# Optimization experiments

Hardware: AMD Instinct MI355X
Metric: run time of the kernel (lower is better)

## Reference

```python
import jax, jax.numpy as jnp
import numpy as np

D = 768
H = 8
HD = D // H
FF = 4 * D


def _linear_params(key, din, dout):
    kw, kb = jax.random.split(key)
    lim = 1.0 / np.sqrt(din)
    W = jax.random.uniform(kw, (din, dout), jnp.float32, -lim, lim)
    b = jax.random.uniform(kb, (dout,), jnp.float32, -lim, lim)
    return W, b


def setup_inputs() -> dict:
    key = jax.random.key(0)
    ks = jax.random.split(key, 8)
    x = jax.random.normal(ks[0], (16, 1024, D), jnp.float32)
    Wq, bq = _linear_params(ks[1], D, D)
    Wk, bk = _linear_params(ks[2], D, D)
    Wv, bv = _linear_params(ks[3], D, D)
    Wo, bo = _linear_params(ks[4], D, D)
    W1, b1 = _linear_params(ks[5], D, FF)
    W2, b2 = _linear_params(ks[6], FF, D)
    gamma = jnp.ones((D,), jnp.float32)
    beta = jnp.zeros((D,), jnp.float32)
    return {"x": x, "gamma": gamma, "beta": beta,
            "Wq": Wq, "bq": bq, "Wk": Wk, "bk": bk, "Wv": Wv, "bv": bv,
            "Wo": Wo, "bo": bo, "W1": W1, "b1": b1, "W2": W2, "b2": b2}


def _layernorm(x, gamma, beta, eps=1e-5):
    mu = jnp.mean(x, axis=-1, keepdims=True)
    var = jnp.var(x, axis=-1, keepdims=True)
    return (x - mu) * jax.lax.rsqrt(var + eps) * gamma + beta


def _block(x, gamma, beta, Wq, bq, Wk, bk, Wv, bv, Wo, bo, W1, b1, W2, b2):
    b, n, d = x.shape
    residual = x
    h = _layernorm(x, gamma, beta)
    # QKV projections -> [b, h, n, hd]
    q = (h @ Wq + bq).reshape(b, n, H, HD).transpose(0, 2, 1, 3)
    k = (h @ Wk + bk).reshape(b, n, H, HD).transpose(0, 2, 1, 3)
    v = (h @ Wv + bv).reshape(b, n, H, HD).transpose(0, 2, 1, 3)
    scale = HD ** 0.5
    scores = jnp.einsum('bhid,bhjd->bhij', q, k) / scale
    attn = jax.nn.softmax(scores, axis=-1)
    out = jnp.einsum('bhij,bhjd->bhid', attn, v)
    out = out.transpose(0, 2, 1, 3).reshape(b, n, d)
    out = out @ Wo + bo
    out = out + residual
    residual = out
    h = _layernorm(out, gamma, beta)  # same LN params reused (as in source)
    h = jax.nn.gelu(h @ W1 + b1, approximate=False)
    h = h @ W2 + b2
    return h + residual


def reference(x, gamma, beta, Wq, bq, Wk, bk, Wv, bv, Wo, bo, W1, b1, W2, b2):
    return _block(x, gamma, beta, Wq, bq, Wk, bk, Wv, bv, Wo, bo, W1, b1, W2, b2)
```

## Files before the change

kernel.cpp:

```cpp
#include <hip/hip_runtime.h>

typedef unsigned short u16;
typedef float f32x4 __attribute__((ext_vector_type(4)));
typedef __bf16 bf16x8 __attribute__((ext_vector_type(8)));

#define AS1 __attribute__((address_space(1)))
#define AS3 __attribute__((address_space(3)))

__device__ __forceinline__ float bf2f(u16 h) {
  return __uint_as_float(((unsigned)h) << 16);
}
__device__ __forceinline__ u16 f2bf(float f) {
  unsigned u = __float_as_uint(f);
  unsigned r = (u + 0x7FFFu + ((u >> 16) & 1u)) >> 16;
  return (u16)r;
}
__device__ __forceinline__ void gload16(const u16* g, u16* l) {
  __builtin_amdgcn_global_load_lds((const AS1 void*)g, (AS3 void*)l, 16, 0, 0);
}

__global__ void transpose_k(const float* __restrict__ in, u16* __restrict__ out,
                            int R, int C) {
  __shared__ u16 t[32][33];
  int c0 = blockIdx.x * 32, r0 = blockIdx.y * 32;
  int tx = threadIdx.x & 31, ty = threadIdx.x >> 5;
  for (int i = 0; i < 32; i += 8)
    t[ty + i][tx] = f2bf(in[(size_t)(r0 + ty + i) * C + c0 + tx]);
  __syncthreads();
  for (int i = 0; i < 32; i += 8)
    out[(size_t)(c0 + ty + i) * R + r0 + tx] = t[tx][ty + i];
}

__global__ void vtrans_k(const u16* __restrict__ v, u16* __restrict__ vt) {
  __shared__ u16 t[32][33];
  int bh = blockIdx.z, b = bh >> 3, h = bh & 7;
  int n0 = blockIdx.y * 32, d0 = blockIdx.x * 32;
  int tx = threadIdx.x & 31, ty = threadIdx.x >> 5;
  const u16* src = v + (size_t)(b * 1024) * 768 + h * 96;
  for (int i = 0; i < 32; i += 8)
    t[ty + i][tx] = src[(size_t)(n0 + ty + i) * 768 + d0 + tx];
  __syncthreads();
  u16* dst = vt + ((size_t)bh * 96 + d0) * 1024 + n0;
  for (int i = 0; i < 32; i += 8)
    dst[(size_t)(ty + i) * 1024 + tx] = t[tx][ty + i];
}

__global__ __launch_bounds__(256) void ln_f32_k(const float* __restrict__ x,
                                                const float* __restrict__ gamma,
                                                const float* __restrict__ beta,
                                                u16* __restrict__ out) {
  __shared__ float red[8];
  int row = blockIdx.x, t = threadIdx.x;
  const float* xr = x + (size_t)row * 768;
  float v[3], s = 0.f, s2 = 0.f;
#pragma unroll
  for (int i = 0; i < 3; i++) {
    v[i] = xr[t + i * 256];
    s += v[i]; s2 += v[i] * v[i];
  }
#pragma unroll
  for (int off = 1; off < 64; off <<= 1) {
    s += __shfl_xor(s, off, 64);
    s2 += __shfl_xor(s2, off, 64);
  }
  int w = t >> 6;
  if ((t & 63) == 0) { red[w] = s; red[4 + w] = s2; }
  __syncthreads();
  s = red[0] + red[1] + red[2] + red[3];
  s2 = red[4] + red[5] + red[6] + red[7];
  float mu = s * (1.f / 768.f);
  float var = s2 * (1.f / 768.f) - mu * mu;
  float rs = rsqrtf(var + 1e-5f);
  u16* orow = out + (size_t)row * 768;
#pragma unroll
  for (int i = 0; i < 3; i++) {
    int c = t + i * 256;
    orow[c] = f2bf((v[i] - mu) * rs * gamma[c] + beta[c]);
  }
}

#define BM 128
#define BN 128
#define BK 32

template <int EPI>
__global__ __launch_bounds__(256, 2) void gemm_bt(
    const u16* __restrict__ A, const u16* __restrict__ Bt,
    const float* __restrict__ bias, const float* __restrict__ res,
    void* __restrict__ Cv, int M, int N, int K) {
  __shared__ u16 As[BM * BK];
  __shared__ u16 Bs[BN * BK];
  int tid = threadIdx.x, lane = tid & 63, w = tid >> 6;
  int l15 = lane & 15, quad = lane >> 4;
  int wm = (w >> 1) * 64, wn = (w & 1) * 64;
  int m0 = blockIdx.x * BM, n0 = blockIdx.y * BN;
  f32x4 acc[4][4] = {};
  for (int k0 = 0; k0 < K; k0 += BK) {
    __syncthreads();
#pragma unroll
    for (int i = 0; i < 2; i++) {
      int c = w * 2 + i;
      int e = c * 512 + lane * 8;
      int r = e >> 5, col = e & 31;
      gload16(A + (size_t)(m0 + r) * K + k0 + col, As + c * 512);
      gload16(Bt + (size_t)(n0 + r) * K + k0 + col, Bs + c * 512);
    }
    __syncthreads();
    bf16x8 af[4], bfv[4];
#pragma unroll
    for (int i = 0; i < 4; i++) {
      af[i] = *(const bf16x8*)(As + (wm + i * 16 + l15) * BK + quad * 8);
      bfv[i] = *(const bf16x8*)(Bs + (wn + i * 16 + l15) * BK + quad * 8);
    }
#pragma unroll
    for (int mt = 0; mt < 4; mt++)
#pragma unroll
      for (int nt = 0; nt < 4; nt++)
        acc[mt][nt] = __builtin_amdgcn_mfma_f32_16x16x32_bf16(
            af[mt], bfv[nt], acc[mt][nt], 0, 0, 0);
  }
#pragma unroll
  for (int nt = 0; nt < 4; nt++) {
    int col = n0 + wn + nt * 16 + l15;
    float bv = bias[col];
#pragma unroll
    for (int mt = 0; mt < 4; mt++) {
      int row = m0 + wm + mt * 16 + quad * 4;
#pragma unroll
      for (int r = 0; r < 4; r++) {
        float v = acc[mt][nt][r] + bv;
        size_t idx = (size_t)(row + r) * N + col;
        if (EPI == 4) {
          v += res[idx];
          ((float*)Cv)[idx] = v;
        } else {
          if (EPI == 2) v = 0.5f * v * (1.0f + erff(v * 0.70710678118654752f));
          ((u16*)Cv)[idx] = f2bf(v);
        }
      }
    }
  }
}

#define QSS 104
#define VSS 72
#define PSS 72
__global__ __launch_bounds__(256, 2) void attn_k(const u16* __restrict__ q,
                                                 const u16* __restrict__ k,
                                                 const u16* __restrict__ vt,
                                                 u16* __restrict__ o) {
  __shared__ u16 qs[64 * QSS];
  __shared__ u16 ks[64 * QSS];
  __shared__ u16 vts[96 * VSS];
  __shared__ u16 ps[4 * 16 * PSS];
  int tid = threadIdx.x, lane = tid & 63, w = tid >> 6;
  int l15 = lane & 15, quad = lane >> 4;
  int qt = blockIdx.x, bh = blockIdx.y;
  int b = bh >> 3, h = bh & 7;
  const u16* qbase = q + (size_t)(b * 1024 + qt * 64) * 768 + h * 96;
  const u16* kbase = k + (size_t)(b * 1024) * 768 + h * 96;
  const u16* vtbase = vt + (size_t)bh * 96 * 1024;
  for (int c = tid; c < 768; c += 256) {
    int r = c / 12, off = (c % 12) * 8;
    *(uint4*)(qs + r * QSS + off) = *(const uint4*)(qbase + (size_t)r * 768 + off);
  }
  float mi[4], li[4];
#pragma unroll
  for (int r = 0; r < 4; r++) { mi[r] = -1e30f; li[r] = 0.f; }
  f32x4 oacc[6] = {};
  const float scale = 0.10206207261596577f;
  for (int kt = 0; kt < 16; kt++) {
    __syncthreads();
    for (int c = tid; c < 768; c += 256) {
      int r = c / 12, off = (c % 12) * 8;
      *(uint4*)(ks + r * QSS + off) =
          *(const uint4*)(kbase + (size_t)(kt * 64 + r) * 768 + off);
    }
    for (int c = tid; c < 768; c += 256) {
      int r = c >> 3, off = (c & 7) * 8;
      *(uint4*)(vts + r * VSS + off) =
          *(const uint4*)(vtbase + (size_t)r * 1024 + kt * 64 + off);
    }
    __syncthreads();
    f32x4 s[4] = {};
#pragma unroll
    for (int kk = 0; kk < 3; kk++) {
      bf16x8 a = *(const bf16x8*)(qs + (w * 16 + l15) * QSS + kk * 32 + quad * 8);
#pragma unroll
      for (int nt = 0; nt < 4; nt++) {
        bf16x8 bb = *(const bf16x8*)(ks + (nt * 16 + l15) * QSS + kk * 32 + quad * 8);
        s[nt] = __builtin_amdgcn_mfma_f32_16x16x32_bf16(a, bb, s[nt], 0, 0, 0);
      }
    }
#pragma unroll
    for (int r = 0; r < 4; r++) {
      float sv[4], mx = -1e30f;
#pragma unroll
      for (int nt = 0; nt < 4; nt++) {
        sv[nt] = s[nt][r] * scale;
        mx = fmaxf(mx, sv[nt]);
      }
#pragma unroll
      for (int off = 1; off < 16; off <<= 1) mx = fmaxf(mx, __shfl_xor(mx, off, 16));
      float mnew = fmaxf(mi[r], mx);
      float alpha = __expf(mi[r] - mnew);
      float rs = 0.f;
#pragma unroll
      for (int nt = 0; nt < 4; nt++) { sv[nt] = __expf(sv[nt] - mnew); rs += sv[nt]; }
#pragma unroll
      for (int off = 1; off < 16; off <<= 1) rs += __shfl_xor(rs, off, 16);
      li[r] = li[r] * alpha + rs;
      mi[r] = mnew;
#pragma unroll
      for (int ht = 0; ht < 6; ht++) oacc[ht][r] *= alpha;
      int prow = quad * 4 + r;
#pragma unroll
      for (int nt = 0; nt < 4; nt++)
        ps[w * 16 * PSS + prow * PSS + nt * 16 + l15] = f2bf(sv[nt]);
    }
    __syncthreads();
#pragma unroll
    for (int kk = 0; kk < 2; kk++) {
      bf16x8 a = *(const bf16x8*)(ps + w * 16 * PSS + l15 * PSS + kk * 32 + quad * 8);
#pragma unroll
      for (int ht = 0; ht < 6; ht++) {
        bf16x8 bb = *(const bf16x8*)(vts + (ht * 16 + l15) * VSS + kk * 32 + quad * 8);
        oacc[ht] = __builtin_amdgcn_mfma_f32_16x16x32_bf16(a, bb, oacc[ht], 0, 0, 0);
      }
    }
  }
  u16* obase = o + (size_t)(b * 1024 + qt * 64 + w * 16) * 768 + h * 96;
#pragma unroll
  for (int r = 0; r < 4; r++) {
    float inv = 1.0f / li[r];
    int row = quad * 4 + r;
#pragma unroll
    for (int ht = 0; ht < 6; ht++)
      obase[(size_t)row * 768 + ht * 16 + l15] = f2bf(oacc[ht][r] * inv);
  }
}

extern "C" void kernel_launch(void* const* d_in, const int* in_sizes, int n_in,
                              void* d_out, int out_size, void* d_ws,
                              size_t ws_size, hipStream_t stream) {
  const float* x = (const float*)d_in[0];
  const float* gamma = (const float*)d_in[1];
  const float* beta = (const float*)d_in[2];
  const float* Wq = (const float*)d_in[3];
  const float* bq = (const float*)d_in[4];
  const float* Wk = (const float*)d_in[5];
  const float* bk = (const float*)d_in[6];
  const float* Wv = (const float*)d_in[7];
  const float* bv = (const float*)d_in[8];
  const float* Wo = (const float*)d_in[9];
  const float* bo = (const float*)d_in[10];
  const float* W1 = (const float*)d_in[11];
  const float* b1 = (const float*)d_in[12];
  const float* W2 = (const float*)d_in[13];
  const float* b2 = (const float*)d_in[14];
  float* out = (float*)d_out;

  char* ws = (char*)d_ws;
  size_t off = 0;
  auto alloc = [&](size_t elems) {
    u16* p = (u16*)(ws + off);
    off += elems * sizeof(u16);
    return p;
  };
  u16* WqT = alloc(768 * 768);
  u16* WkT = alloc(768 * 768);
  u16* WvT = alloc(768 * 768);
  u16* WoT = alloc(768 * 768);
  u16* W1T = alloc((size_t)768 * 3072);
  u16* W2T = alloc((size_t)3072 * 768);
  u16* hb = alloc((size_t)16384 * 768);
  u16* qb = alloc((size_t)16384 * 768);
  u16* kb = alloc((size_t)16384 * 768);
  u16* vb = alloc((size_t)16384 * 768);

  transpose_k<<<dim3(24, 24), 256, 0, stream>>>(Wq, WqT, 768, 768);
  transpose_k<<<dim3(24, 24), 256, 0, stream>>>(Wk, WkT, 768, 768);
  transpose_k<<<dim3(24, 24), 256, 0, stream>>>(Wv, WvT, 768, 768);
  transpose_k<<<dim3(24, 24), 256, 0, stream>>>(Wo, WoT, 768, 768);
  transpose_k<<<dim3(96, 24), 256, 0, stream>>>(W1, W1T, 768, 3072);
  transpose_k<<<dim3(24, 96), 256, 0, stream>>>(W2, W2T, 3072, 768);

  ln_f32_k<<<16384, 256, 0, stream>>>(x, gamma, beta, hb);
  gemm_bt<0><<<dim3(128, 6), 256, 0, stream>>>(hb, WqT, bq, nullptr, qb,
                                               16384, 768, 768);
  gemm_bt<0><<<dim3(128, 6), 256, 0, stream>>>(hb, WkT, bk, nullptr, kb,
                                               16384, 768, 768);
  gemm_bt<0><<<dim3(128, 6), 256, 0, stream>>>(hb, WvT, bv, nullptr, vb,
                                               16384, 768, 768);
  vtrans_k<<<dim3(3, 32, 128), 256, 0, stream>>>(vb, hb);
  attn_k<<<dim3(16, 128), 256, 0, stream>>>(qb, kb, hb, vb);
  gemm_bt<4><<<dim3(128, 6), 256, 0, stream>>>(vb, WoT, bo, x, out,
                                               16384, 768, 768);
  ln_f32_k<<<16384, 256, 0, stream>>>(out, gamma, beta, kb);
  for (int c = 0; c < 4; c++) {
    const u16* h2c = kb + (size_t)c * 4096 * 768;
    const float* y1c = out + (size_t)c * 4096 * 768;
    float* outc = out + (size_t)c * 4096 * 768;
    gemm_bt<2><<<dim3(32, 24), 256, 0, stream>>>(h2c, W1T, b1, nullptr, vb,
                                                 4096, 3072, 768);
    gemm_bt<4><<<dim3(32, 6), 256, 0, stream>>>(vb, W2T, b2, y1c, outc,
                                                4096, 768, 3072);
  }
}
```

Baseline: 904.6 us.

## Double-buffer K/V tiles in attention with register prefetch

The attention kernel now prefetches the next K and V^T tile into registers while computing on the current tile, then writes them into a second LDS buffer at the end of the iteration. This overlaps global-load latency with the MFMA and softmax work and cuts the barriers per iteration from three to one. The barrier between writing P and reading it is replaced by an LDS wait, relying on each wave reading only its own P rows. LDS use rises from about 40KB to about 66KB per block, which may exceed what two blocks per CU can share and lower occupancy. The last iteration also issues a redundant wrapped-around load.

After: 858.2 us. 1.05x faster.

```diff
diff --git a/kernel.cpp b/kernel.cpp
--- a/kernel.cpp
+++ b/kernel.cpp
@@ -150,8 +150,8 @@
                                                  const u16* __restrict__ vt,
                                                  u16* __restrict__ o) {
   __shared__ u16 qs[64 * QSS];
-  __shared__ u16 ks[64 * QSS];
-  __shared__ u16 vts[96 * VSS];
+  __shared__ u16 ks[2][64 * QSS];
+  __shared__ u16 vts[2][96 * VSS];
   __shared__ u16 ps[4 * 16 * PSS];
   int tid = threadIdx.x, lane = tid & 63, w = tid >> 6;
   int l15 = lane & 15, quad = lane >> 4;
@@ -160,35 +160,51 @@
   const u16* qbase = q + (size_t)(b * 1024 + qt * 64) * 768 + h * 96;
   const u16* kbase = k + (size_t)(b * 1024) * 768 + h * 96;
   const u16* vtbase = vt + (size_t)bh * 96 * 1024;
-  for (int c = tid; c < 768; c += 256) {
-    int r = c / 12, off = (c % 12) * 8;
-    *(uint4*)(qs + r * QSS + off) = *(const uint4*)(qbase + (size_t)r * 768 + off);
-  }
+  int kr[3], ko[3], vr[3], vo[3];
+#pragma unroll
+  for (int i = 0; i < 3; i++) {
+    int c = tid + i * 256;
+    kr[i] = c / 12; ko[i] = (c % 12) * 8;
+    vr[i] = c >> 3; vo[i] = (c & 7) * 8;
+  }
+#pragma unroll
+  for (int i = 0; i < 3; i++)
+    *(uint4*)(qs + kr[i] * QSS + ko[i]) =
+        *(const uint4*)(qbase + (size_t)kr[i] * 768 + ko[i]);
+  uint4 kreg[3], vreg[3];
+#pragma unroll
+  for (int i = 0; i < 3; i++) {
+    kreg[i] = *(const uint4*)(kbase + (size_t)kr[i] * 768 + ko[i]);
+    vreg[i] = *(const uint4*)(vtbase + (size_t)vr[i] * 1024 + vo[i]);
+  }
+#pragma unroll
+  for (int i = 0; i < 3; i++) {
+    *(uint4*)(ks[0] + kr[i] * QSS + ko[i]) = kreg[i];
+    *(uint4*)(vts[0] + vr[i] * VSS + vo[i]) = vreg[i];
+  }
+  __syncthreads();
+
   float mi[4], li[4];
 #pragma unroll
   for (int r = 0; r < 4; r++) { mi[r] = -1e30f; li[r] = 0.f; }
   f32x4 oacc[6] = {};
   const float scale = 0.10206207261596577f;
   for (int kt = 0; kt < 16; kt++) {
-    __syncthreads();
-    for (int c = tid; c < 768; c += 256) {
-      int r = c / 12, off = (c % 12) * 8;
-      *(uint4*)(ks + r * QSS + off) =
-          *(const uint4*)(kbase + (size_t)(kt * 64 + r) * 768 + off);
-    }
-    for (int c = tid; c < 768; c += 256) {
-      int r = c >> 3, off = (c & 7) * 8;
-      *(uint4*)(vts + r * VSS + off) =
-          *(const uint4*)(vtbase + (size_t)r * 1024 + kt * 64 + off);
-    }
-    __syncthreads();
+    int cur = kt & 1, nxt = cur ^ 1;
+    int ktn = (kt + 1) & 15;
+#pragma unroll
+    for (int i = 0; i < 3; i++) {
+      kreg[i] = *(const uint4*)(kbase + (size_t)(ktn * 64 + kr[i]) * 768 + ko[i]);
+      vreg[i] = *(const uint4*)(vtbase + (size_t)vr[i] * 1024 + ktn * 64 + vo[i]);
+    }
     f32x4 s[4] = {};
 #pragma unroll
     for (int kk = 0; kk < 3; kk++) {
       bf16x8 a = *(const bf16x8*)(qs + (w * 16 + l15) * QSS + kk * 32 + quad * 8);
 #pragma unroll
       for (int nt = 0; nt < 4; nt++) {
-        bf16x8 bb = *(const bf16x8*)(ks + (nt * 16 + l15) * QSS + kk * 32 + quad * 8);
+        bf16x8 bb =
+            *(const bf16x8*)(ks[cur] + (nt * 16 + l15) * QSS + kk * 32 + quad * 8);
         s[nt] = __builtin_amdgcn_mfma_f32_16x16x32_bf16(a, bb, s[nt], 0, 0, 0);
       }
     }
@@ -218,16 +234,23 @@
       for (int nt = 0; nt < 4; nt++)
         ps[w * 16 * PSS + prow * PSS + nt * 16 + l15] = f2bf(sv[nt]);
     }
-    __syncthreads();
+    asm volatile("s_waitcnt lgkmcnt(0)" ::: "memory");
 #pragma unroll
     for (int kk = 0; kk < 2; kk++) {
       bf16x8 a = *(const bf16x8*)(ps + w * 16 * PSS + l15 * PSS + kk * 32 + quad * 8);
 #pragma unroll
       for (int ht = 0; ht < 6; ht++) {
-        bf16x8 bb = *(const bf16x8*)(vts + (ht * 16 + l15) * VSS + kk * 32 + quad * 8);
+        bf16x8 bb =
+            *(const bf16x8*)(vts[cur] + (ht * 16 + l15) * VSS + kk * 32 + quad * 8);
         oacc[ht] = __builtin_amdgcn_mfma_f32_16x16x32_bf16(a, bb, oacc[ht], 0, 0, 0);
       }
     }
+#pragma unroll
+    for (int i = 0; i < 3; i++) {
+      *(uint4*)(ks[nxt] + kr[i] * QSS + ko[i]) = kreg[i];
+      *(uint4*)(vts[nxt] + vr[i] * VSS + vo[i]) = vreg[i];
+    }
+    __syncthreads();
   }
   u16* obase = o + (size_t)(b * 1024 + qt * 64 + w * 16) * 768 + h * 96;
 #pragma unroll
```
